# Performance work log

Hardware: AMD Instinct MI355X
Metric: run time of the kernel (lower is better)

Reference implementation:

```python
import jax, jax.numpy as jnp
import numpy as np

D_MODEL = 1024
D_FF = 4096
NUM_EXPERTS = 8
TOP_K = 2
SEQ = 1024
BATCH = 2


def setup_inputs() -> dict:
    key = jax.random.key(0)
    ks = jax.random.split(key, 7)
    s = 0.02
    x = jax.random.normal(ks[0], (SEQ, BATCH, D_MODEL), dtype=jnp.float32)
    gate_w = jax.random.normal(ks[1], (D_MODEL, NUM_EXPERTS), dtype=jnp.float32) * s
    gate_b = jnp.zeros((NUM_EXPERTS,), dtype=jnp.float32)
    W1 = jax.random.normal(ks[2], (NUM_EXPERTS, D_MODEL, D_FF), dtype=jnp.float32) * s
    b1 = jnp.zeros((NUM_EXPERTS, D_FF), dtype=jnp.float32)
    W2 = jax.random.normal(ks[3], (NUM_EXPERTS, D_FF, D_MODEL), dtype=jnp.float32) * s
    b2 = jnp.zeros((NUM_EXPERTS, D_MODEL), dtype=jnp.float32)
    return {"x": x, "gate_w": gate_w, "gate_b": gate_b,
            "W1": W1, "b1": b1, "W2": W2, "b2": b2}


def reference(x, gate_w, gate_b, W1, b1, W2, b2):
    S, B, D = x.shape
    x_flat = x.reshape(-1, D)                       # [T, D], T = S*B
    scores = x_flat @ gate_w + gate_b               # [T, E]
    topk_vals, topk_idx = jax.lax.top_k(scores, TOP_K)   # [T, K]
    topk_probs = jax.nn.softmax(topk_vals, axis=-1)      # [T, K]
    # combine weight per (token, expert): sum of probs over slots routed to e
    one_hot = jax.nn.one_hot(topk_idx, NUM_EXPERTS, dtype=x.dtype)  # [T, K, E]
    combine = jnp.einsum('tk,tke->te', topk_probs, one_hot)         # [T, E]
    # dense per-expert FFN (tokens with combine weight 0 contribute nothing,
    # matching the masked gather/scatter in the torch loop)
    h = jax.nn.relu(jnp.einsum('td,edf->etf', x_flat, W1) + b1[:, None, :])  # [E, T, F]
    y = jnp.einsum('etf,efd->etd', h, W2) + b2[:, None, :]                    # [E, T, D]
    out = jnp.einsum('te,etd->td', combine, y)       # [T, D]
    return out.reshape(S, B, D)
```

## Files before the change

kernel.cpp:

```cpp
#include <hip/hip_runtime.h>
#include <stdint.h>

#define T_TOKENS 2048
#define DM 1024
#define DF 4096
#define NEXP 8
#define NSLOTS (T_TOKENS * 2)

typedef __bf16 bf16x8 __attribute__((ext_vector_type(8)));
typedef float f32x4 __attribute__((ext_vector_type(4)));

__device__ __forceinline__ ushort f2bf(float f) {
    union { float f; uint32_t u; } v; v.f = f;
    uint32_t r = v.u + 0x7FFFu + ((v.u >> 16) & 1u);
    return (ushort)(r >> 16);
}

__device__ __forceinline__ void gload16(const ushort* g, ushort* l) {
    __builtin_amdgcn_global_load_lds(
        (const __attribute__((address_space(1))) uint32_t*)g,
        (__attribute__((address_space(3))) uint32_t*)l,
        16, 0, 0);
}

__global__ void init_cnt(uint32_t* cnt) {
    if (threadIdx.x < NEXP) cnt[threadIdx.x] = 0;
}

__global__ __launch_bounds__(256) void gate_route(
    const float* __restrict__ x, const float* __restrict__ gw,
    const float* __restrict__ gb,
    uint32_t* __restrict__ route, uint32_t* __restrict__ cnt,
    float* __restrict__ prob, uint32_t* __restrict__ epk)
{
    const int w = threadIdx.x >> 6;
    const int lane = threadIdx.x & 63;
    const int t = blockIdx.x * 4 + w;
    float acc[NEXP];
#pragma unroll
    for (int e = 0; e < NEXP; ++e) acc[e] = 0.f;
    const float* xr = x + (size_t)t * DM;
#pragma unroll
    for (int j = 0; j < DM / 64; ++j) {
        const int d = j * 64 + lane;
        const float xv = xr[d];
        const float* g = gw + (size_t)d * NEXP;
#pragma unroll
        for (int e = 0; e < NEXP; ++e) acc[e] += xv * g[e];
    }
#pragma unroll
    for (int e = 0; e < NEXP; ++e) {
#pragma unroll
        for (int off = 32; off > 0; off >>= 1)
            acc[e] += __shfl_xor(acc[e], off);
        acc[e] += gb[e];
    }
    if (lane == 0) {
        int e0 = 0; float v0 = acc[0];
#pragma unroll
        for (int e = 1; e < NEXP; ++e) if (acc[e] > v0) { v0 = acc[e]; e0 = e; }
        int e1 = -1; float v1 = -1e30f;
#pragma unroll
        for (int e = 0; e < NEXP; ++e) if (e != e0 && acc[e] > v1) { v1 = acc[e]; e1 = e; }
        const float ex = expf(v1 - v0);
        const float inv = 1.f / (1.f + ex);
        prob[t * 2 + 0] = inv;
        prob[t * 2 + 1] = ex * inv;
        uint32_t pos = atomicAdd(&cnt[e0], 1u);
        route[e0 * T_TOKENS + pos] = (uint32_t)(t * 2);
        epk[t * 2] = ((uint32_t)e0 << 16) | pos;
        pos = atomicAdd(&cnt[e1], 1u);
        route[e1 * T_TOKENS + pos] = (uint32_t)(t * 2 + 1);
        epk[t * 2 + 1] = ((uint32_t)e1 << 16) | pos;
    }
}

__global__ void prefix_offs(const uint32_t* __restrict__ cnt,
                            uint32_t* __restrict__ offs)
{
    if (threadIdx.x == 0) {
        uint32_t a = 0;
#pragma unroll
        for (int e = 0; e < NEXP; ++e) { offs[e] = a; a += cnt[e]; }
        offs[NEXP] = a;
    }
}

__global__ __launch_bounds__(256) void convert_x(const float* __restrict__ x,
                                                 ushort* __restrict__ xb)
{
    const int i = (blockIdx.x * 256 + threadIdx.x) * 4;
    const float4 v = *reinterpret_cast<const float4*>(x + i);
    ushort4 o;
    o.x = f2bf(v.x); o.y = f2bf(v.y); o.z = f2bf(v.z); o.w = f2bf(v.w);
    *reinterpret_cast<ushort4*>(xb + i) = o;
}

template<int K, int N>
__global__ __launch_bounds__(256) void conv_transpose(const float* __restrict__ W,
                                                      ushort* __restrict__ Wb)
{
    const int e  = blockIdx.y;
    const int nt = blockIdx.x % (N / 64);
    const int kt = blockIdx.x / (N / 64);
    const int k0 = kt * 64, n0 = nt * 64;
    __shared__ ushort T[64][80];
    const int t = threadIdx.x;
    const int kr = t >> 4, nc = (t & 15) * 4;
    const float* src = W + ((size_t)e * K + k0 + kr) * N + n0 + nc;
#pragma unroll
    for (int i = 0; i < 4; ++i) {
        const float4 v = *reinterpret_cast<const float4*>(src + (size_t)i * 16 * N);
        T[nc + 0][kr + i * 16] = f2bf(v.x);
        T[nc + 1][kr + i * 16] = f2bf(v.y);
        T[nc + 2][kr + i * 16] = f2bf(v.z);
        T[nc + 3][kr + i * 16] = f2bf(v.w);
    }
    __syncthreads();
    const int r = t >> 2, c0 = t & 3;
    ushort* dst = Wb + ((size_t)e * N + n0 + r) * K + k0;
#pragma unroll
    for (int i = 0; i < 2; ++i) {
        const int c = c0 + i * 4;
        const uint4 v = *reinterpret_cast<const uint4*>(&T[r][c * 8]);
        *reinterpret_cast<uint4*>(dst + c * 8) = v;
    }
}

template<int KD, int ND, bool FIRST, int SPLIT, int NMT, int NT>
__global__ __launch_bounds__(256, 4) void moe_gemm10(
    const ushort* __restrict__ Abuf,
    const ushort* __restrict__ Wb,
    const float* __restrict__ bias,
    const uint32_t* __restrict__ route,
    const uint32_t* __restrict__ cnt,
    const uint32_t* __restrict__ offs,
    const float* __restrict__ prob,
    ushort* __restrict__ hout,
    float* __restrict__ yout)
{
    const int bx0 = blockIdx.x;
    const int cpx = (NEXP * NMT * NT) >> 3;
    const int wk  = (bx0 & 7) * cpx + (bx0 >> 3);
    const int e   = wk / (NMT * NT);
    const int r   = wk % (NMT * NT);
    const int nt  = r / NMT;
    const int mt  = r % NMT;
    const uint32_t cntE = cnt[e];
    const int m0 = mt * 128;
    if ((uint32_t)m0 >= cntE) return;
    const uint32_t hb = offs[e];
    const int n0 = nt * 128;
    const int z  = (SPLIT > 1) ? (int)blockIdx.z : 0;
    const int kbeg = z * (KD / SPLIT);
    const int niter = (KD / SPLIT) / 32;

    __shared__ ushort As[2][128 * 32];
    __shared__ ushort Bs[2][128 * 32];
    __shared__ uint32_t s_route[128];
    __shared__ float s_p[128];

    const int tid = threadIdx.x;
    if (FIRST) {
        if (tid < 128) {
            const uint32_t idx = (uint32_t)(m0 + tid);
            const uint32_t s = (idx < cntE) ? route[e * T_TOKENS + idx] : 0u;
            s_route[tid] = s;
            s_p[tid] = prob[s];
        }
        __syncthreads();
    }

    const int w = tid >> 6, l = tid & 63;

    const ushort* asrc[2];
    const ushort* bsrc[2];
#pragma unroll
    for (int i = 0; i < 2; ++i) {
        const int chunk = (w * 2 + i) * 64 + l;
        const int row = chunk >> 2;
        const int c   = chunk & 3;
        const int cs  = c ^ ((row >> 1) & 3);
        size_t arow;
        if (FIRST) arow = (size_t)(s_route[row] >> 1);
        else       arow = (size_t)(hb + m0 + row);
        asrc[i] = Abuf + arow * KD + cs * 8 + kbeg;
        bsrc[i] = Wb + ((size_t)e * ND + n0 + row) * KD + cs * 8 + kbeg;
    }

    f32x4 acc[4][4];
#pragma unroll
    for (int i = 0; i < 4; ++i)
#pragma unroll
        for (int j = 0; j < 4; ++j) acc[i][j] = (f32x4){0.f, 0.f, 0.f, 0.f};

    const int q = l & 15, g = l >> 4;
    const int wm = w >> 1, wn = w & 1;

    int aoff[4], boff[4];
#pragma unroll
    for (int mi = 0; mi < 4; ++mi) {
        int row = wm * 64 + mi * 16 + q;
        aoff[mi] = row * 64 + (g ^ ((row >> 1) & 3)) * 16;
        row = wn * 64 + mi * 16 + q;
        boff[mi] = row * 64 + (g ^ ((row >> 1) & 3)) * 16;
    }

    ushort* const abase0 = &As[0][0];
    ushort* const bbase0 = &Bs[0][0];

#pragma unroll
    for (int i = 0; i < 2; ++i) gload16(asrc[i], abase0 + (w * 2 + i) * 512);
#pragma unroll
    for (int i = 0; i < 2; ++i) gload16(bsrc[i], bbase0 + (w * 2 + i) * 512);

    int cur = 0;
    for (int t = 0; t < niter; ++t) {
        if (t + 1 < niter) {
            ushort* ad = abase0 + (cur ^ 1) * (128 * 32) + (w * 2) * 512;
            ushort* bd = bbase0 + (cur ^ 1) * (128 * 32) + (w * 2) * 512;
            const int k1 = (t + 1) * 32;
#pragma unroll
            for (int i = 0; i < 2; ++i) gload16(asrc[i] + k1, ad + i * 512);
#pragma unroll
            for (int i = 0; i < 2; ++i) gload16(bsrc[i] + k1, bd + i * 512);
            asm volatile("s_waitcnt vmcnt(4)" ::: "memory");
        } else {
            asm volatile("s_waitcnt vmcnt(0)" ::: "memory");
        }
        __builtin_amdgcn_s_barrier();
        __builtin_amdgcn_sched_barrier(0);

        const char* Ab = (const char*)(abase0 + cur * (128 * 32));
        const char* Bb = (const char*)(bbase0 + cur * (128 * 32));
        bf16x8 af[4], bv[4];
#pragma unroll
        for (int mi = 0; mi < 4; ++mi)
            af[mi] = *reinterpret_cast<const bf16x8*>(Ab + aoff[mi]);
#pragma unroll
        for (int ni = 0; ni < 4; ++ni)
            bv[ni] = *reinterpret_cast<const bf16x8*>(Bb + boff[ni]);
        __builtin_amdgcn_s_setprio(1);
#pragma unroll
        for (int mi = 0; mi < 4; ++mi)
#pragma unroll
            for (int ni = 0; ni < 4; ++ni)
                acc[mi][ni] = __builtin_amdgcn_mfma_f32_16x16x32_bf16(
                    af[mi], bv[ni], acc[mi][ni], 0, 0, 0);
        __builtin_amdgcn_s_setprio(0);
        __builtin_amdgcn_s_barrier();
        cur ^= 1;
    }

#pragma unroll
    for (int mi = 0; mi < 4; ++mi) {
#pragma unroll
        for (int ni = 0; ni < 4; ++ni) {
            const int gcol = n0 + wn * 64 + ni * 16 + q;
#pragma unroll
            for (int j = 0; j < 4; ++j) {
                const int row = wm * 64 + mi * 16 + g * 4 + j;
                if ((uint32_t)(m0 + row) < cntE) {
                    const size_t grow = (size_t)(hb + m0 + row);
                    if (FIRST) {
                        float v = acc[mi][ni][j] + bias[e * ND + gcol];
                        v = fmaxf(v, 0.f) * s_p[row];
                        hout[grow * ND + gcol] = f2bf(v);
                    } else {
                        yout[((size_t)z * NSLOTS + grow) * ND + gcol] = acc[mi][ni][j];
                    }
                }
            }
        }
    }
}

__global__ __launch_bounds__(256) void combine5(
    const float* __restrict__ yc, const uint32_t* __restrict__ epk,
    const uint32_t* __restrict__ offs, const float* __restrict__ prob,
    const float* __restrict__ b2, float* __restrict__ out)
{
    const int gid = blockIdx.x * 256 + threadIdx.x;
    const int t = gid >> 8;
    const int dq = gid & 255;
    const uint32_t p0 = epk[2 * t], p1 = epk[2 * t + 1];
    const uint32_t e0 = p0 >> 16, e1 = p1 >> 16;
    const uint32_t r0 = offs[e0] + (p0 & 0xFFFFu);
    const uint32_t r1 = offs[e1] + (p1 & 0xFFFFu);
    const float w0 = prob[2 * t], w1 = prob[2 * t + 1];
    const float4 bb0 = reinterpret_cast<const float4*>(b2 + (size_t)e0 * DM)[dq];
    const float4 bb1 = reinterpret_cast<const float4*>(b2 + (size_t)e1 * DM)[dq];
    float4 o = { w0 * bb0.x + w1 * bb1.x, w0 * bb0.y + w1 * bb1.y,
                 w0 * bb0.z + w1 * bb1.z, w0 * bb0.w + w1 * bb1.w };
    const float4* Y = reinterpret_cast<const float4*>(yc);
#pragma unroll
    for (int zz = 0; zz < 4; ++zz) {
        const float4 a = Y[((size_t)zz * NSLOTS + r0) * 256 + dq];
        const float4 b = Y[((size_t)zz * NSLOTS + r1) * 256 + dq];
        o.x += a.x + b.x; o.y += a.y + b.y; o.z += a.z + b.z; o.w += a.w + b.w;
    }
    reinterpret_cast<float4*>(out)[gid] = o;
}

template<int KD, int ND, bool FIRST>
__global__ __launch_bounds__(256) void moe_gemm_v1(
    const ushort* __restrict__ Abuf, const float* __restrict__ W,
    const float* __restrict__ bias, const uint32_t* __restrict__ route,
    const uint32_t* __restrict__ cnt, const float* __restrict__ prob,
    ushort* __restrict__ hout, float* __restrict__ yout)
{
    const int e = blockIdx.x >> 4;
    const int mt = blockIdx.x & 15;
    const uint32_t cntE = cnt[e];
    const int m0 = mt * 128;
    if ((uint32_t)m0 >= cntE) return;
    const int n0 = blockIdx.y * 128;
    const int tid = threadIdx.x;
    __shared__ ushort Asm[128][40];
    __shared__ ushort Bsm[128][40];
    __shared__ uint32_t s_route[128];
    if (tid < 128) {
        const uint32_t idx = (uint32_t)(m0 + tid);
        s_route[tid] = (idx < cntE) ? route[e * T_TOKENS + idx] : 0xFFFFFFFFu;
    }
    __syncthreads();
    const int ar = tid >> 1, ah = tid & 1;
    const uint32_t s_a = s_route[ar];
    size_t arow = 0;
    if (s_a != 0xFFFFFFFFu) arow = FIRST ? (size_t)(s_a >> 1) : (size_t)s_a;
    const ushort* asrc = Abuf + arow * KD + ah * 16;
    const int c4 = tid & 31, kq = tid >> 5;
    const float* wbase = W + (size_t)e * KD * ND + (size_t)n0 + (size_t)c4 * 4;
    f32x4 acc[4][4];
#pragma unroll
    for (int i = 0; i < 4; ++i)
#pragma unroll
        for (int j = 0; j < 4; ++j) acc[i][j] = (f32x4){0.f, 0.f, 0.f, 0.f};
    const int lane = tid & 63, wv = tid >> 6;
    const int wm = wv >> 1, wn = wv & 1;
    const int q = lane & 15, g = lane >> 4;
    for (int k0 = 0; k0 < KD; k0 += 32) {
        {
            const uint4* src = reinterpret_cast<const uint4*>(asrc + k0);
            const uint4 v0 = src[0];
            const uint4 v1 = src[1];
            *reinterpret_cast<uint4*>(&Asm[ar][ah * 16]) = v0;
            *reinterpret_cast<uint4*>(&Asm[ar][ah * 16 + 8]) = v1;
        }
        {
            ushort vals[4][4];
#pragma unroll
            for (int r = 0; r < 4; ++r) {
                const float4 v = *reinterpret_cast<const float4*>(
                    wbase + (size_t)(k0 + kq * 4 + r) * ND);
                vals[r][0] = f2bf(v.x); vals[r][1] = f2bf(v.y);
                vals[r][2] = f2bf(v.z); vals[r][3] = f2bf(v.w);
            }
#pragma unroll
            for (int c = 0; c < 4; ++c) {
                const ushort4 o = { vals[0][c], vals[1][c], vals[2][c], vals[3][c] };
                *reinterpret_cast<ushort4*>(&Bsm[c4 * 4 + c][kq * 4]) = o;
            }
        }
        __syncthreads();
        bf16x8 af[4], bfr[4];
#pragma unroll
        for (int mi = 0; mi < 4; ++mi)
            af[mi] = *reinterpret_cast<const bf16x8*>(&Asm[wm * 64 + mi * 16 + q][g * 8]);
#pragma unroll
        for (int ni = 0; ni < 4; ++ni)
            bfr[ni] = *reinterpret_cast<const bf16x8*>(&Bsm[wn * 64 + ni * 16 + q][g * 8]);
#pragma unroll
        for (int mi = 0; mi < 4; ++mi)
#pragma unroll
            for (int ni = 0; ni < 4; ++ni)
                acc[mi][ni] = __builtin_amdgcn_mfma_f32_16x16x32_bf16(
                    af[mi], bfr[ni], acc[mi][ni], 0, 0, 0);
        __syncthreads();
    }
#pragma unroll
    for (int mi = 0; mi < 4; ++mi) {
#pragma unroll
        for (int ni = 0; ni < 4; ++ni) {
            const int gcol = n0 + wn * 64 + ni * 16 + q;
#pragma unroll
            for (int j = 0; j < 4; ++j) {
                const int row = wm * 64 + mi * 16 + g * 4 + j;
                if ((uint32_t)(m0 + row) < cntE) {
                    const uint32_t s = s_route[row];
                    float v = acc[mi][ni][j] + bias[e * ND + gcol];
                    if (FIRST) {
                        v = fmaxf(v, 0.f);
                        hout[(size_t)s * ND + gcol] = f2bf(v);
                    } else {
                        yout[(size_t)s * ND + gcol] = v * prob[s];
                    }
                }
            }
        }
    }
}

__global__ __launch_bounds__(256) void combine1(const float* __restrict__ yc,
                                                float* __restrict__ out)
{
    const int gid = blockIdx.x * 256 + threadIdx.x;
    const int t = gid >> 8;
    const int dq = gid & 255;
    const float4 va = reinterpret_cast<const float4*>(yc)[(size_t)(2 * t) * 256 + dq];
    const float4 vb = reinterpret_cast<const float4*>(yc)[(size_t)(2 * t + 1) * 256 + dq];
    const float4 o = { va.x + vb.x, va.y + vb.y, va.z + vb.z, va.w + vb.w };
    reinterpret_cast<float4*>(out)[gid] = o;
}

extern "C" void kernel_launch(void* const* d_in, const int* in_sizes, int n_in,
                              void* d_out, int out_size, void* d_ws, size_t ws_size,
                              hipStream_t stream)
{
    const float* x  = (const float*)d_in[0];
    const float* gw = (const float*)d_in[1];
    const float* gb = (const float*)d_in[2];
    const float* W1 = (const float*)d_in[3];
    const float* b1 = (const float*)d_in[4];
    const float* W2 = (const float*)d_in[5];
    const float* b2 = (const float*)d_in[6];
    float* out = (float*)d_out;
    char* ws = (char*)d_ws;

    const size_t OFF_XB    = 0;
    const size_t OFF_H     = 4194304;
    const size_t OFF_ROUTE = 38797312;
    const size_t OFF_CNT   = 38862848;
    const size_t OFF_OFFS  = 38862912;
    const size_t OFF_PROB  = 38862976;
    const size_t OFF_EPK   = 38879360;
    const size_t OFF_W1B   = 41943040;
    const size_t OFF_W2B   = 109051904;
    const size_t OFF_YC    = OFF_W1B;
    const size_t NEED      = 176160768ull;

    if (ws_size >= NEED) {
        ushort*   xb    = (ushort*)(ws + OFF_XB);
        ushort*   h     = (ushort*)(ws + OFF_H);
        float*    yc    = (float*)(ws + OFF_YC);
        uint32_t* route = (uint32_t*)(ws + OFF_ROUTE);
        uint32_t* cnt   = (uint32_t*)(ws + OFF_CNT);
        uint32_t* offs  = (uint32_t*)(ws + OFF_OFFS);
        float*    prob  = (float*)(ws + OFF_PROB);
        uint32_t* epk   = (uint32_t*)(ws + OFF_EPK);
        ushort*   w1b   = (ushort*)(ws + OFF_W1B);
        ushort*   w2b   = (ushort*)(ws + OFF_W2B);

        hipLaunchKernelGGL(init_cnt, dim3(1), dim3(64), 0, stream, cnt);
        hipLaunchKernelGGL(gate_route, dim3(T_TOKENS / 4), dim3(256), 0, stream,
                           x, gw, gb, route, cnt, prob, epk);
        hipLaunchKernelGGL(prefix_offs, dim3(1), dim3(64), 0, stream, cnt, offs);
        hipLaunchKernelGGL(convert_x, dim3(T_TOKENS * DM / 1024), dim3(256), 0, stream, x, xb);
        hipLaunchKernelGGL((conv_transpose<DM, DF>), dim3((DM / 64) * (DF / 64), NEXP),
                           dim3(256), 0, stream, W1, w1b);
        hipLaunchKernelGGL((moe_gemm10<DM, DF, true, 1, 16, 32>),
                           dim3(NEXP * 16 * 32, 1, 1), dim3(256), 0, stream,
                           xb, w1b, b1, route, cnt, offs, prob, h, (float*)nullptr);
        hipLaunchKernelGGL((conv_transpose<DF, DM>), dim3((DF / 64) * (DM / 64), NEXP),
                           dim3(256), 0, stream, W2, w2b);
        hipLaunchKernelGGL((moe_gemm10<DF, DM, false, 4, 16, 8>),
                           dim3(NEXP * 16 * 8, 1, 4), dim3(256), 0, stream,
                           h, w2b, (const float*)nullptr, route, cnt, offs,
                           (const float*)nullptr, (ushort*)nullptr, yc);
        hipLaunchKernelGGL(combine5, dim3(T_TOKENS * DM / 1024), dim3(256), 0, stream,
                           yc, epk, offs, prob, b2, out);
    } else {
        const size_t F_XB = 0, F_H = 4194304, F_YC = 37748736;
        const size_t F_ROUTE = 54525952, F_CNT = 54591488, F_PROB = 54591552;
        ushort*   xb    = (ushort*)(ws + F_XB);
        ushort*   h     = (ushort*)(ws + F_H);
        float*    yc    = (float*)(ws + F_YC);
        uint32_t* route = (uint32_t*)(ws + F_ROUTE);
        uint32_t* cnt   = (uint32_t*)(ws + F_CNT);
        float*    prob  = (float*)(ws + F_PROB);
        uint32_t* epk   = (uint32_t*)(ws + F_PROB + 16384);

        hipLaunchKernelGGL(init_cnt, dim3(1), dim3(64), 0, stream, cnt);
        hipLaunchKernelGGL(gate_route, dim3(T_TOKENS / 4), dim3(256), 0, stream,
                           x, gw, gb, route, cnt, prob, epk);
        hipLaunchKernelGGL(convert_x, dim3(T_TOKENS * DM / 1024), dim3(256), 0, stream, x, xb);
        hipLaunchKernelGGL((moe_gemm_v1<DM, DF, true>), dim3(NEXP * 16, DF / 128),
                           dim3(256), 0, stream, xb, W1, b1, route, cnt, prob,
                           h, (float*)nullptr);
        hipLaunchKernelGGL((moe_gemm_v1<DF, DM, false>), dim3(NEXP * 16, DM / 128),
                           dim3(256), 0, stream, h, W2, b2, route, cnt, prob,
                           (ushort*)nullptr, yc);
        hipLaunchKernelGGL(combine1, dim3(T_TOKENS * DM / 1024), dim3(256), 0, stream, yc, out);
    }
}
```

Before: 298.0 us.

## Merge gating, x/W1 conversion into one prep kernel; overlap W2 transpose with GEMM1

Gating/routing, the x-to-bf16 conversion and the W1 convert-transpose now run as one heterogeneous prep kernel whose block ranges are dispatched by block index. The W2 convert-transpose blocks are appended to the first expert GEMM's grid so they can fill idle compute units while GEMM1 runs. This removes several launches and the serialization between independent preprocessing stages. The cost is a larger shared-memory footprint for the mixed kernel, possible occupancy interference with the GEMM blocks, and transpose blocks that each loop over four k-tiles.

```diff
diff --git a/kernel.cpp b/kernel.cpp
--- a/kernel.cpp
+++ b/kernel.cpp
@@ -27,54 +27,6 @@
     if (threadIdx.x < NEXP) cnt[threadIdx.x] = 0;
 }
 
-__global__ __launch_bounds__(256) void gate_route(
-    const float* __restrict__ x, const float* __restrict__ gw,
-    const float* __restrict__ gb,
-    uint32_t* __restrict__ route, uint32_t* __restrict__ cnt,
-    float* __restrict__ prob, uint32_t* __restrict__ epk)
-{
-    const int w = threadIdx.x >> 6;
-    const int lane = threadIdx.x & 63;
-    const int t = blockIdx.x * 4 + w;
-    float acc[NEXP];
-#pragma unroll
-    for (int e = 0; e < NEXP; ++e) acc[e] = 0.f;
-    const float* xr = x + (size_t)t * DM;
-#pragma unroll
-    for (int j = 0; j < DM / 64; ++j) {
-        const int d = j * 64 + lane;
-        const float xv = xr[d];
-        const float* g = gw + (size_t)d * NEXP;
-#pragma unroll
-        for (int e = 0; e < NEXP; ++e) acc[e] += xv * g[e];
-    }
-#pragma unroll
-    for (int e = 0; e < NEXP; ++e) {
-#pragma unroll
-        for (int off = 32; off > 0; off >>= 1)
-            acc[e] += __shfl_xor(acc[e], off);
-        acc[e] += gb[e];
-    }
-    if (lane == 0) {
-        int e0 = 0; float v0 = acc[0];
-#pragma unroll
-        for (int e = 1; e < NEXP; ++e) if (acc[e] > v0) { v0 = acc[e]; e0 = e; }
-        int e1 = -1; float v1 = -1e30f;
-#pragma unroll
-        for (int e = 0; e < NEXP; ++e) if (e != e0 && acc[e] > v1) { v1 = acc[e]; e1 = e; }
-        const float ex = expf(v1 - v0);
-        const float inv = 1.f / (1.f + ex);
-        prob[t * 2 + 0] = inv;
-        prob[t * 2 + 1] = ex * inv;
-        uint32_t pos = atomicAdd(&cnt[e0], 1u);
-        route[e0 * T_TOKENS + pos] = (uint32_t)(t * 2);
-        epk[t * 2] = ((uint32_t)e0 << 16) | pos;
-        pos = atomicAdd(&cnt[e1], 1u);
-        route[e1 * T_TOKENS + pos] = (uint32_t)(t * 2 + 1);
-        epk[t * 2 + 1] = ((uint32_t)e1 << 16) | pos;
-    }
-}
-
 __global__ void prefix_offs(const uint32_t* __restrict__ cnt,
                             uint32_t* __restrict__ offs)
 {
@@ -86,44 +38,257 @@
     }
 }
 
-__global__ __launch_bounds__(256) void convert_x(const float* __restrict__ x,
-                                                 ushort* __restrict__ xb)
-{
-    const int i = (blockIdx.x * 256 + threadIdx.x) * 4;
-    const float4 v = *reinterpret_cast<const float4*>(x + i);
-    ushort4 o;
-    o.x = f2bf(v.x); o.y = f2bf(v.y); o.z = f2bf(v.z); o.w = f2bf(v.w);
-    *reinterpret_cast<ushort4*>(xb + i) = o;
-}
-
-template<int K, int N>
-__global__ __launch_bounds__(256) void conv_transpose(const float* __restrict__ W,
-                                                      ushort* __restrict__ Wb)
-{
-    const int e  = blockIdx.y;
-    const int nt = blockIdx.x % (N / 64);
-    const int kt = blockIdx.x / (N / 64);
-    const int k0 = kt * 64, n0 = nt * 64;
+__global__ __launch_bounds__(256) void prep_kernel(
+    const float* __restrict__ x, const float* __restrict__ gw,
+    const float* __restrict__ gb, const float* __restrict__ W1,
+    uint32_t* __restrict__ route, uint32_t* __restrict__ cnt,
+    float* __restrict__ prob, uint32_t* __restrict__ epk,
+    ushort* __restrict__ xb, ushort* __restrict__ w1b)
+{
     __shared__ ushort T[64][80];
-    const int t = threadIdx.x;
-    const int kr = t >> 4, nc = (t & 15) * 4;
-    const float* src = W + ((size_t)e * K + k0 + kr) * N + n0 + nc;
-#pragma unroll
-    for (int i = 0; i < 4; ++i) {
-        const float4 v = *reinterpret_cast<const float4*>(src + (size_t)i * 16 * N);
-        T[nc + 0][kr + i * 16] = f2bf(v.x);
-        T[nc + 1][kr + i * 16] = f2bf(v.y);
-        T[nc + 2][kr + i * 16] = f2bf(v.z);
-        T[nc + 3][kr + i * 16] = f2bf(v.w);
-    }
-    __syncthreads();
-    const int r = t >> 2, c0 = t & 3;
-    ushort* dst = Wb + ((size_t)e * N + n0 + r) * K + k0;
-#pragma unroll
-    for (int i = 0; i < 2; ++i) {
-        const int c = c0 + i * 4;
-        const uint4 v = *reinterpret_cast<const uint4*>(&T[r][c * 8]);
-        *reinterpret_cast<uint4*>(dst + c * 8) = v;
+    const int bx = blockIdx.x;
+    const int tid = threadIdx.x;
+
+    if (bx < 512) {
+        const int w = tid >> 6;
+        const int lane = tid & 63;
+        const int t = bx * 4 + w;
+        float acc[NEXP];
+#pragma unroll
+        for (int e = 0; e < NEXP; ++e) acc[e] = 0.f;
+        const float* xr = x + (size_t)t * DM;
+#pragma unroll
+        for (int j = 0; j < DM / 64; ++j) {
+            const int d = j * 64 + lane;
+            const float xv = xr[d];
+            const float* g = gw + (size_t)d * NEXP;
+#pragma unroll
+            for (int e = 0; e < NEXP; ++e) acc[e] += xv * g[e];
+        }
+#pragma unroll
+        for (int e = 0; e < NEXP; ++e) {
+#pragma unroll
+            for (int off = 32; off > 0; off >>= 1)
+                acc[e] += __shfl_xor(acc[e], off);
+            acc[e] += gb[e];
+        }
+        if (lane == 0) {
+            int e0 = 0; float v0 = acc[0];
+#pragma unroll
+            for (int e = 1; e < NEXP; ++e) if (acc[e] > v0) { v0 = acc[e]; e0 = e; }
+            int e1 = -1; float v1 = -1e30f;
+#pragma unroll
+            for (int e = 0; e < NEXP; ++e) if (e != e0 && acc[e] > v1) { v1 = acc[e]; e1 = e; }
+            const float ex = expf(v1 - v0);
+            const float inv = 1.f / (1.f + ex);
+            prob[t * 2 + 0] = inv;
+            prob[t * 2 + 1] = ex * inv;
+            uint32_t pos = atomicAdd(&cnt[e0], 1u);
+            route[e0 * T_TOKENS + pos] = (uint32_t)(t * 2);
+            epk[t * 2] = ((uint32_t)e0 << 16) | pos;
+            pos = atomicAdd(&cnt[e1], 1u);
+            route[e1 * T_TOKENS + pos] = (uint32_t)(t * 2 + 1);
+            epk[t * 2 + 1] = ((uint32_t)e1 << 16) | pos;
+        }
+    } else if (bx < 2560) {
+        const int i = ((bx - 512) * 256 + tid) * 4;
+        const float4 v = *reinterpret_cast<const float4*>(x + i);
+        ushort4 o;
+        o.x = f2bf(v.x); o.y = f2bf(v.y); o.z = f2bf(v.z); o.w = f2bf(v.w);
+        *reinterpret_cast<ushort4*>(xb + i) = o;
+    } else {
+        const int rel = bx - 2560;
+        const int e   = rel >> 8;
+        const int r   = rel & 255;
+        const int nt  = r & 63;
+        const int ktg = r >> 6;
+        const int kr  = tid >> 4, nc = (tid & 15) * 4;
+        const int rr  = tid >> 2, c0 = tid & 3;
+        for (int kk = 0; kk < 4; ++kk) {
+            const int k0 = ktg * 256 + kk * 64;
+            const int n0 = nt * 64;
+            const float* src = W1 + ((size_t)e * DM + k0 + kr) * DF + n0 + nc;
+#pragma unroll
+            for (int i2 = 0; i2 < 4; ++i2) {
+                const float4 v = *reinterpret_cast<const float4*>(src + (size_t)i2 * 16 * DF);
+                T[nc + 0][kr + i2 * 16] = f2bf(v.x);
+                T[nc + 1][kr + i2 * 16] = f2bf(v.y);
+                T[nc + 2][kr + i2 * 16] = f2bf(v.z);
+                T[nc + 3][kr + i2 * 16] = f2bf(v.w);
+            }
+            __syncthreads();
+            ushort* dst = w1b + ((size_t)e * DF + n0 + rr) * DM + k0;
+#pragma unroll
+            for (int i2 = 0; i2 < 2; ++i2) {
+                const int c = c0 + i2 * 4;
+                *reinterpret_cast<uint4*>(dst + c * 8) =
+                    *reinterpret_cast<const uint4*>(&T[rr][c * 8]);
+            }
+            __syncthreads();
+        }
+    }
+}
+
+__global__ __launch_bounds__(256, 4) void gemm1_trw2(
+    const ushort* __restrict__ xb, const ushort* __restrict__ w1b,
+    const float* __restrict__ b1, const uint32_t* __restrict__ route,
+    const uint32_t* __restrict__ cnt, const uint32_t* __restrict__ offs,
+    const float* __restrict__ prob, ushort* __restrict__ hout,
+    const float* __restrict__ W2, ushort* __restrict__ w2b)
+{
+    __shared__ __attribute__((aligned(16))) char smem[33792];
+    const int bx0 = blockIdx.x;
+    const int tid = threadIdx.x;
+
+    if (bx0 < 4096) {
+        ushort* Asm = (ushort*)smem;
+        ushort* Bsm = (ushort*)(smem + 16384);
+        uint32_t* s_route = (uint32_t*)(smem + 32768);
+        float* s_p = (float*)(smem + 33280);
+
+        const int cpx = (NEXP * 16 * 32) >> 3;
+        const int wk  = (bx0 & 7) * cpx + (bx0 >> 3);
+        const int e   = wk / (16 * 32);
+        const int r   = wk % (16 * 32);
+        const int nt  = r / 16;
+        const int mt  = r % 16;
+        const uint32_t cntE = cnt[e];
+        const int m0 = mt * 128;
+        if ((uint32_t)m0 >= cntE) return;
+        const uint32_t hb = offs[e];
+        const int n0 = nt * 128;
+        const int niter = DM / 32;
+
+        if (tid < 128) {
+            const uint32_t idx = (uint32_t)(m0 + tid);
+            const uint32_t s = (idx < cntE) ? route[e * T_TOKENS + idx] : 0u;
+            s_route[tid] = s;
+            s_p[tid] = prob[s];
+        }
+        __syncthreads();
+
+        const int w = tid >> 6, l = tid & 63;
+        const ushort* asrc[2];
+        const ushort* bsrc[2];
+#pragma unroll
+        for (int i = 0; i < 2; ++i) {
+            const int chunk = (w * 2 + i) * 64 + l;
+            const int row = chunk >> 2;
+            const int c   = chunk & 3;
+            const int cs  = c ^ ((row >> 1) & 3);
+            const size_t arow = (size_t)(s_route[row] >> 1);
+            asrc[i] = xb + arow * DM + cs * 8;
+            bsrc[i] = w1b + ((size_t)e * DF + n0 + row) * DM + cs * 8;
+        }
+
+        f32x4 acc[4][4];
+#pragma unroll
+        for (int i = 0; i < 4; ++i)
+#pragma unroll
+            for (int j = 0; j < 4; ++j) acc[i][j] = (f32x4){0.f, 0.f, 0.f, 0.f};
+
+        const int q = l & 15, g = l >> 4;
+        const int wm = w >> 1, wn = w & 1;
+        int aoff[4], boff[4];
+#pragma unroll
+        for (int mi = 0; mi < 4; ++mi) {
+            int row = wm * 64 + mi * 16 + q;
+            aoff[mi] = row * 64 + (g ^ ((row >> 1) & 3)) * 16;
+            row = wn * 64 + mi * 16 + q;
+            boff[mi] = row * 64 + (g ^ ((row >> 1) & 3)) * 16;
+        }
+
+#pragma unroll
+        for (int i = 0; i < 2; ++i) gload16(asrc[i], Asm + (w * 2 + i) * 512);
+#pragma unroll
+        for (int i = 0; i < 2; ++i) gload16(bsrc[i], Bsm + (w * 2 + i) * 512);
+
+        int cur = 0;
+        for (int t = 0; t < niter; ++t) {
+            if (t + 1 < niter) {
+                ushort* ad = Asm + (cur ^ 1) * (128 * 32) + (w * 2) * 512;
+                ushort* bd = Bsm + (cur ^ 1) * (128 * 32) + (w * 2) * 512;
+                const int k1 = (t + 1) * 32;
+#pragma unroll
+                for (int i = 0; i < 2; ++i) gload16(asrc[i] + k1, ad + i * 512);
+#pragma unroll
+                for (int i = 0; i < 2; ++i) gload16(bsrc[i] + k1, bd + i * 512);
+                asm volatile("s_waitcnt vmcnt(4)" ::: "memory");
+            } else {
+                asm volatile("s_waitcnt vmcnt(0)" ::: "memory");
+            }
+            __builtin_amdgcn_s_barrier();
+            __builtin_amdgcn_sched_barrier(0);
+
+            const char* Ab = (const char*)(Asm + cur * (128 * 32));
+            const char* Bb = (const char*)(Bsm + cur * (128 * 32));
+            bf16x8 af[4], bv[4];
+#pragma unroll
+            for (int mi = 0; mi < 4; ++mi)
+                af[mi] = *reinterpret_cast<const bf16x8*>(Ab + aoff[mi]);
+#pragma unroll
+            for (int ni = 0; ni < 4; ++ni)
+                bv[ni] = *reinterpret_cast<const bf16x8*>(Bb + boff[ni]);
+            __builtin_amdgcn_s_setprio(1);
+#pragma unroll
+            for (int mi = 0; mi < 4; ++mi)
+#pragma unroll
+                for (int ni = 0; ni < 4; ++ni)
+                    acc[mi][ni] = __builtin_amdgcn_mfma_f32_16x16x32_bf16(
+                        af[mi], bv[ni], acc[mi][ni], 0, 0, 0);
+            __builtin_amdgcn_s_setprio(0);
+            __builtin_amdgcn_s_barrier();
+            cur ^= 1;
+        }
+
+#pragma unroll
+        for (int mi = 0; mi < 4; ++mi) {
+#pragma unroll
+            for (int ni = 0; ni < 4; ++ni) {
+                const int gcol = n0 + wn * 64 + ni * 16 + q;
+#pragma unroll
+                for (int j = 0; j < 4; ++j) {
+                    const int row = wm * 64 + mi * 16 + g * 4 + j;
+                    if ((uint32_t)(m0 + row) < cntE) {
+                        const size_t grow = (size_t)(hb + m0 + row);
+                        float v = acc[mi][ni][j] + b1[e * DF + gcol];
+                        v = fmaxf(v, 0.f) * s_p[row];
+                        hout[grow * DF + gcol] = f2bf(v);
+                    }
+                }
+            }
+        }
+    } else {
+        ushort (*T)[80] = reinterpret_cast<ushort(*)[80]>(smem);
+        const int rel = bx0 - 4096;
+        const int e   = rel >> 8;
+        const int r   = rel & 255;
+        const int nt  = r & 15;
+        const int ktg = r >> 4;
+        const int kr  = tid >> 4, nc = (tid & 15) * 4;
+        const int rr  = tid >> 2, c0 = tid & 3;
+        for (int kk = 0; kk < 4; ++kk) {
+            const int k0 = ktg * 256 + kk * 64;
+            const int n0 = nt * 64;
+            const float* src = W2 + ((size_t)e * DF + k0 + kr) * DM + n0 + nc;
+#pragma unroll
+            for (int i2 = 0; i2 < 4; ++i2) {
+                const float4 v = *reinterpret_cast<const float4*>(src + (size_t)i2 * 16 * DM);
+                T[nc + 0][kr + i2 * 16] = f2bf(v.x);
+                T[nc + 1][kr + i2 * 16] = f2bf(v.y);
+                T[nc + 2][kr + i2 * 16] = f2bf(v.z);
+                T[nc + 3][kr + i2 * 16] = f2bf(v.w);
+            }
+            __syncthreads();
+            ushort* dst = w2b + ((size_t)e * DM + n0 + rr) * DF + k0;
+#pragma unroll
+            for (int i2 = 0; i2 < 2; ++i2) {
+                const int c = c0 + i2 * 4;
+                *reinterpret_cast<uint4*>(dst + c * 8) =
+                    *reinterpret_cast<const uint4*>(&T[rr][c * 8]);
+            }
+            __syncthreads();
+        }
     }
 }
 
@@ -172,7 +337,6 @@
     }
 
     const int w = tid >> 6, l = tid & 63;
-
     const ushort* asrc[2];
     const ushort* bsrc[2];
 #pragma unroll
@@ -196,7 +360,6 @@
 
     const int q = l & 15, g = l >> 4;
     const int wm = w >> 1, wn = w & 1;
-
     int aoff[4], boff[4];
 #pragma unroll
     for (int mi = 0; mi < 4; ++mi) {
@@ -302,6 +465,62 @@
     reinterpret_cast<float4*>(out)[gid] = o;
 }
 
+__global__ __launch_bounds__(256) void gate_route_fb(
+    const float* __restrict__ x, const float* __restrict__ gw,
+    const float* __restrict__ gb,
+    uint32_t* __restrict__ route, uint32_t* __restrict__ cnt,
+    float* __restrict__ prob)
+{
+    const int w = threadIdx.x >> 6;
+    const int lane = threadIdx.x & 63;
+    const int t = blockIdx.x * 4 + w;
+    float acc[NEXP];
+#pragma unroll
+    for (int e = 0; e < NEXP; ++e) acc[e] = 0.f;
+    const float* xr = x + (size_t)t * DM;
+#pragma unroll
+    for (int j = 0; j < DM / 64; ++j) {
+        const int d = j * 64 + lane;
+        const float xv = xr[d];
+        const float* g = gw + (size_t)d * NEXP;
+#pragma unroll
+        for (int e = 0; e < NEXP; ++e) acc[e] += xv * g[e];
+    }
+#pragma unroll
+    for (int e = 0; e < NEXP; ++e) {
+#pragma unroll
+        for (int off = 32; off > 0; off >>= 1)
+            acc[e] += __shfl_xor(acc[e], off);
+        acc[e] += gb[e];
+    }
+    if (lane == 0) {
+        int e0 = 0; float v0 = acc[0];
+#pragma unroll
+        for (int e = 1; e < NEXP; ++e) if (acc[e] > v0) { v0 = acc[e]; e0 = e; }
+        int e1 = -1; float v1 = -1e30f;
+#pragma unroll
+        for (int e = 0; e < NEXP; ++e) if (e != e0 && acc[e] > v1) { v1 = acc[e]; e1 = e; }
+        const float ex = expf(v1 - v0);
+        const float inv = 1.f / (1.f + ex);
+        prob[t * 2 + 0] = inv;
+        prob[t * 2 + 1] = ex * inv;
+        uint32_t pos = atomicAdd(&cnt[e0], 1u);
+        route[e0 * T_TOKENS + pos] = (uint32_t)(t * 2);
+        pos = atomicAdd(&cnt[e1], 1u);
+        route[e1 * T_TOKENS + pos] = (uint32_t)(t * 2 + 1);
+    }
+}
+
+__global__ __launch_bounds__(256) void convert_x_fb(const float* __restrict__ x,
+                                                    ushort* __restrict__ xb)
+{
+    const int i = (blockIdx.x * 256 + threadIdx.x) * 4;
+    const float4 v = *reinterpret_cast<const float4*>(x + i);
+    ushort4 o;
+    o.x = f2bf(v.x); o.y = f2bf(v.y); o.z = f2bf(v.z); o.w = f2bf(v.w);
+    *reinterpret_cast<ushort4*>(xb + i) = o;
+}
+
 template<int KD, int ND, bool FIRST>
 __global__ __launch_bounds__(256) void moe_gemm_v1(
     const ushort* __restrict__ Abuf, const float* __restrict__ W,
@@ -452,17 +671,11 @@
         ushort*   w2b   = (ushort*)(ws + OFF_W2B);
 
         hipLaunchKernelGGL(init_cnt, dim3(1), dim3(64), 0, stream, cnt);
-        hipLaunchKernelGGL(gate_route, dim3(T_TOKENS / 4), dim3(256), 0, stream,
-                           x, gw, gb, route, cnt, prob, epk);
+        hipLaunchKernelGGL(prep_kernel, dim3(4608), dim3(256), 0, stream,
+                           x, gw, gb, W1, route, cnt, prob, epk, xb, w1b);
         hipLaunchKernelGGL(prefix_offs, dim3(1), dim3(64), 0, stream, cnt, offs);
-        hipLaunchKernelGGL(convert_x, dim3(T_TOKENS * DM / 1024), dim3(256), 0, stream, x, xb);
-        hipLaunchKernelGGL((conv_transpose<DM, DF>), dim3((DM / 64) * (DF / 64), NEXP),
-                           dim3(256), 0, stream, W1, w1b);
-        hipLaunchKernelGGL((moe_gemm10<DM, DF, true, 1, 16, 32>),
-                           dim3(NEXP * 16 * 32, 1, 1), dim3(256), 0, stream,
-                           xb, w1b, b1, route, cnt, offs, prob, h, (float*)nullptr);
-        hipLaunchKernelGGL((conv_transpose<DF, DM>), dim3((DF / 64) * (DM / 64), NEXP),
-                           dim3(256), 0, stream, W2, w2b);
+        hipLaunchKernelGGL(gemm1_trw2, dim3(4096 + 2048), dim3(256), 0, stream,
+                           xb, w1b, b1, route, cnt, offs, prob, h, W2, w2b);
         hipLaunchKernelGGL((moe_gemm10<DF, DM, false, 4, 16, 8>),
                            dim3(NEXP * 16 * 8, 1, 4), dim3(256), 0, stream,
                            h, w2b, (const float*)nullptr, route, cnt, offs,
@@ -478,12 +691,11 @@
         uint32_t* route = (uint32_t*)(ws + F_ROUTE);
         uint32_t* cnt   = (uint32_t*)(ws + F_CNT);
         float*    prob  = (float*)(ws + F_PROB);
-        uint32_t* epk   = (uint32_t*)(ws + F_PROB + 16384);
 
         hipLaunchKernelGGL(init_cnt, dim3(1), dim3(64), 0, stream, cnt);
-        hipLaunchKernelGGL(gate_route, dim3(T_TOKENS / 4), dim3(256), 0, stream,
-                           x, gw, gb, route, cnt, prob, epk);
-        hipLaunchKernelGGL(convert_x, dim3(T_TOKENS * DM / 1024), dim3(256), 0, stream, x, xb);
+        hipLaunchKernelGGL(gate_route_fb, dim3(T_TOKENS / 4), dim3(256), 0, stream,
+                           x, gw, gb, route, cnt, prob);
+        hipLaunchKernelGGL(convert_x_fb, dim3(T_TOKENS * DM / 1024), dim3(256), 0, stream, x, xb);
         hipLaunchKernelGGL((moe_gemm_v1<DM, DF, true>), dim3(NEXP * 16, DF / 128),
                            dim3(256), 0, stream, xb, W1, b1, route, cnt, prob,
                            h, (float*)nullptr);
```

Result: faster. 285.9 us (-4.1%).

## Convert fp32 weights to bf16 inside GEMM loaders; fuse gating with x conversion

Applied to the files above, without the earlier changes.

Removes the separate conv_transpose kernels that wrote bf16 transposed copies of W1 and W2. The GEMM now reads the fp32 weights directly, converts and transposes them in registers, and writes them to a padded LDS buffer, prefetching one step ahead. Gate routing and x conversion are merged into one launch. This saves a full read and write of the weights per call, but the GEMM now reads twice as many weight bytes, does conversion work in the inner loop, and replaces the async global-to-LDS copy for B with register staging plus __syncthreads.

```diff
diff --git a/kernel.cpp b/kernel.cpp
--- a/kernel.cpp
+++ b/kernel.cpp
@@ -27,110 +27,81 @@
     if (threadIdx.x < NEXP) cnt[threadIdx.x] = 0;
 }
 
-__global__ __launch_bounds__(256) void gate_route(
+__global__ void prefix_offs(const uint32_t* __restrict__ cnt,
+                            uint32_t* __restrict__ offs)
+{
+    if (threadIdx.x == 0) {
+        uint32_t a = 0;
+#pragma unroll
+        for (int e = 0; e < NEXP; ++e) { offs[e] = a; a += cnt[e]; }
+        offs[NEXP] = a;
+    }
+}
+
+__global__ __launch_bounds__(256) void prep_kernel(
     const float* __restrict__ x, const float* __restrict__ gw,
     const float* __restrict__ gb,
     uint32_t* __restrict__ route, uint32_t* __restrict__ cnt,
-    float* __restrict__ prob, uint32_t* __restrict__ epk)
-{
-    const int w = threadIdx.x >> 6;
-    const int lane = threadIdx.x & 63;
-    const int t = blockIdx.x * 4 + w;
-    float acc[NEXP];
-#pragma unroll
-    for (int e = 0; e < NEXP; ++e) acc[e] = 0.f;
-    const float* xr = x + (size_t)t * DM;
-#pragma unroll
-    for (int j = 0; j < DM / 64; ++j) {
-        const int d = j * 64 + lane;
-        const float xv = xr[d];
-        const float* g = gw + (size_t)d * NEXP;
-#pragma unroll
-        for (int e = 0; e < NEXP; ++e) acc[e] += xv * g[e];
-    }
-#pragma unroll
-    for (int e = 0; e < NEXP; ++e) {
-#pragma unroll
-        for (int off = 32; off > 0; off >>= 1)
-            acc[e] += __shfl_xor(acc[e], off);
-        acc[e] += gb[e];
-    }
-    if (lane == 0) {
-        int e0 = 0; float v0 = acc[0];
-#pragma unroll
-        for (int e = 1; e < NEXP; ++e) if (acc[e] > v0) { v0 = acc[e]; e0 = e; }
-        int e1 = -1; float v1 = -1e30f;
-#pragma unroll
-        for (int e = 0; e < NEXP; ++e) if (e != e0 && acc[e] > v1) { v1 = acc[e]; e1 = e; }
-        const float ex = expf(v1 - v0);
-        const float inv = 1.f / (1.f + ex);
-        prob[t * 2 + 0] = inv;
-        prob[t * 2 + 1] = ex * inv;
-        uint32_t pos = atomicAdd(&cnt[e0], 1u);
-        route[e0 * T_TOKENS + pos] = (uint32_t)(t * 2);
-        epk[t * 2] = ((uint32_t)e0 << 16) | pos;
-        pos = atomicAdd(&cnt[e1], 1u);
-        route[e1 * T_TOKENS + pos] = (uint32_t)(t * 2 + 1);
-        epk[t * 2 + 1] = ((uint32_t)e1 << 16) | pos;
-    }
-}
-
-__global__ void prefix_offs(const uint32_t* __restrict__ cnt,
-                            uint32_t* __restrict__ offs)
-{
-    if (threadIdx.x == 0) {
-        uint32_t a = 0;
-#pragma unroll
-        for (int e = 0; e < NEXP; ++e) { offs[e] = a; a += cnt[e]; }
-        offs[NEXP] = a;
-    }
-}
-
-__global__ __launch_bounds__(256) void convert_x(const float* __restrict__ x,
-                                                 ushort* __restrict__ xb)
-{
-    const int i = (blockIdx.x * 256 + threadIdx.x) * 4;
-    const float4 v = *reinterpret_cast<const float4*>(x + i);
-    ushort4 o;
-    o.x = f2bf(v.x); o.y = f2bf(v.y); o.z = f2bf(v.z); o.w = f2bf(v.w);
-    *reinterpret_cast<ushort4*>(xb + i) = o;
-}
-
-template<int K, int N>
-__global__ __launch_bounds__(256) void conv_transpose(const float* __restrict__ W,
-                                                      ushort* __restrict__ Wb)
-{
-    const int e  = blockIdx.y;
-    const int nt = blockIdx.x % (N / 64);
-    const int kt = blockIdx.x / (N / 64);
-    const int k0 = kt * 64, n0 = nt * 64;
-    __shared__ ushort T[64][80];
-    const int t = threadIdx.x;
-    const int kr = t >> 4, nc = (t & 15) * 4;
-    const float* src = W + ((size_t)e * K + k0 + kr) * N + n0 + nc;
-#pragma unroll
-    for (int i = 0; i < 4; ++i) {
-        const float4 v = *reinterpret_cast<const float4*>(src + (size_t)i * 16 * N);
-        T[nc + 0][kr + i * 16] = f2bf(v.x);
-        T[nc + 1][kr + i * 16] = f2bf(v.y);
-        T[nc + 2][kr + i * 16] = f2bf(v.z);
-        T[nc + 3][kr + i * 16] = f2bf(v.w);
-    }
-    __syncthreads();
-    const int r = t >> 2, c0 = t & 3;
-    ushort* dst = Wb + ((size_t)e * N + n0 + r) * K + k0;
-#pragma unroll
-    for (int i = 0; i < 2; ++i) {
-        const int c = c0 + i * 4;
-        const uint4 v = *reinterpret_cast<const uint4*>(&T[r][c * 8]);
-        *reinterpret_cast<uint4*>(dst + c * 8) = v;
+    float* __restrict__ prob, uint32_t* __restrict__ epk,
+    ushort* __restrict__ xb)
+{
+    const int bx = blockIdx.x;
+    const int tid = threadIdx.x;
+
+    if (bx < 512) {
+        const int w = tid >> 6;
+        const int lane = tid & 63;
+        const int t = bx * 4 + w;
+        float acc[NEXP];
+#pragma unroll
+        for (int e = 0; e < NEXP; ++e) acc[e] = 0.f;
+        const float* xr = x + (size_t)t * DM;
+#pragma unroll
+        for (int j = 0; j < DM / 64; ++j) {
+            const int d = j * 64 + lane;
+            const float xv = xr[d];
+            const float* g = gw + (size_t)d * NEXP;
+#pragma unroll
+            for (int e = 0; e < NEXP; ++e) acc[e] += xv * g[e];
+        }
+#pragma unroll
+        for (int e = 0; e < NEXP; ++e) {
+#pragma unroll
+            for (int off = 32; off > 0; off >>= 1)
+                acc[e] += __shfl_xor(acc[e], off);
+            acc[e] += gb[e];
+        }
+        if (lane == 0) {
+            int e0 = 0; float v0 = acc[0];
+#pragma unroll
+            for (int e = 1; e < NEXP; ++e) if (acc[e] > v0) { v0 = acc[e]; e0 = e; }
+            int e1 = -1; float v1 = -1e30f;
+#pragma unroll
+            for (int e = 0; e < NEXP; ++e) if (e != e0 && acc[e] > v1) { v1 = acc[e]; e1 = e; }
+            const float ex = expf(v1 - v0);
+            const float inv = 1.f / (1.f + ex);
+            prob[t * 2 + 0] = inv;
+            prob[t * 2 + 1] = ex * inv;
+            uint32_t pos = atomicAdd(&cnt[e0], 1u);
+            route[e0 * T_TOKENS + pos] = (uint32_t)(t * 2);
+            epk[t * 2] = ((uint32_t)e0 << 16) | pos;
+            pos = atomicAdd(&cnt[e1], 1u);
+            route[e1 * T_TOKENS + pos] = (uint32_t)(t * 2 + 1);
+            epk[t * 2 + 1] = ((uint32_t)e1 << 16) | pos;
+        }
+    } else {
+        const int i = ((bx - 512) * 256 + tid) * 4;
+        const float4 v = *reinterpret_cast<const float4*>(x + i);
+        ushort4 o;
+        o.x = f2bf(v.x); o.y = f2bf(v.y); o.z = f2bf(v.z); o.w = f2bf(v.w);
+        *reinterpret_cast<ushort4*>(xb + i) = o;
     }
 }
 
 template<int KD, int ND, bool FIRST, int SPLIT, int NMT, int NT>
-__global__ __launch_bounds__(256, 4) void moe_gemm10(
+__global__ __launch_bounds__(256, 4) void moe_gemm12(
     const ushort* __restrict__ Abuf,
-    const ushort* __restrict__ Wb,
+    const float* __restrict__ W,
     const float* __restrict__ bias,
     const uint32_t* __restrict__ route,
     const uint32_t* __restrict__ cnt,
@@ -156,7 +127,7 @@
     const int niter = (KD / SPLIT) / 32;
 
     __shared__ ushort As[2][128 * 32];
-    __shared__ ushort Bs[2][128 * 32];
+    __shared__ ushort Bs[2][128 * 40];
     __shared__ uint32_t s_route[128];
     __shared__ float s_p[128];
 
@@ -174,7 +145,6 @@
     const int w = tid >> 6, l = tid & 63;
 
     const ushort* asrc[2];
-    const ushort* bsrc[2];
 #pragma unroll
     for (int i = 0; i < 2; ++i) {
         const int chunk = (w * 2 + i) * 64 + l;
@@ -185,8 +155,13 @@
         if (FIRST) arow = (size_t)(s_route[row] >> 1);
         else       arow = (size_t)(hb + m0 + row);
         asrc[i] = Abuf + arow * KD + cs * 8 + kbeg;
-        bsrc[i] = Wb + ((size_t)e * ND + n0 + row) * KD + cs * 8 + kbeg;
-    }
+    }
+
+    const int c4 = tid & 31;
+    const int kq = tid >> 5;
+    const float* wbase = W + ((size_t)e * KD + kbeg + (size_t)kq * 4) * ND
+                         + n0 + c4 * 4;
+    ushort* const bdst0 = &Bs[0][0];
 
     f32x4 acc[4][4];
 #pragma unroll
@@ -203,36 +178,47 @@
         int row = wm * 64 + mi * 16 + q;
         aoff[mi] = row * 64 + (g ^ ((row >> 1) & 3)) * 16;
         row = wn * 64 + mi * 16 + q;
-        boff[mi] = row * 64 + (g ^ ((row >> 1) & 3)) * 16;
+        boff[mi] = row * 40 + g * 8;
     }
 
     ushort* const abase0 = &As[0][0];
-    ushort* const bbase0 = &Bs[0][0];
-
-#pragma unroll
-    for (int i = 0; i < 2; ++i) gload16(asrc[i], abase0 + (w * 2 + i) * 512);
-#pragma unroll
-    for (int i = 0; i < 2; ++i) gload16(bsrc[i], bbase0 + (w * 2 + i) * 512);
+
+    {
+        float4 b0 = *reinterpret_cast<const float4*>(wbase + (size_t)0 * ND);
+        float4 b1 = *reinterpret_cast<const float4*>(wbase + (size_t)1 * ND);
+        float4 b2 = *reinterpret_cast<const float4*>(wbase + (size_t)2 * ND);
+        float4 b3 = *reinterpret_cast<const float4*>(wbase + (size_t)3 * ND);
+#pragma unroll
+        for (int i = 0; i < 2; ++i) gload16(asrc[i], abase0 + (w * 2 + i) * 512);
+        const int bn = c4 * 4;
+        ushort4 o0 = { f2bf(b0.x), f2bf(b1.x), f2bf(b2.x), f2bf(b3.x) };
+        ushort4 o1 = { f2bf(b0.y), f2bf(b1.y), f2bf(b2.y), f2bf(b3.y) };
+        ushort4 o2 = { f2bf(b0.z), f2bf(b1.z), f2bf(b2.z), f2bf(b3.z) };
+        ushort4 o3 = { f2bf(b0.w), f2bf(b1.w), f2bf(b2.w), f2bf(b3.w) };
+        *reinterpret_cast<ushort4*>(bdst0 + (bn + 0) * 40 + kq * 4) = o0;
+        *reinterpret_cast<ushort4*>(bdst0 + (bn + 1) * 40 + kq * 4) = o1;
+        *reinterpret_cast<ushort4*>(bdst0 + (bn + 2) * 40 + kq * 4) = o2;
+        *reinterpret_cast<ushort4*>(bdst0 + (bn + 3) * 40 + kq * 4) = o3;
+    }
+    __syncthreads();
 
     int cur = 0;
     for (int t = 0; t < niter; ++t) {
-        if (t + 1 < niter) {
+        float4 b0, b1, b2, b3;
+        const bool pf = (t + 1 < niter);
+        if (pf) {
+            const size_t k1 = (size_t)(t + 1) * 32;
+            b0 = *reinterpret_cast<const float4*>(wbase + (k1 + 0) * ND);
+            b1 = *reinterpret_cast<const float4*>(wbase + (k1 + 1) * ND);
+            b2 = *reinterpret_cast<const float4*>(wbase + (k1 + 2) * ND);
+            b3 = *reinterpret_cast<const float4*>(wbase + (k1 + 3) * ND);
             ushort* ad = abase0 + (cur ^ 1) * (128 * 32) + (w * 2) * 512;
-            ushort* bd = bbase0 + (cur ^ 1) * (128 * 32) + (w * 2) * 512;
-            const int k1 = (t + 1) * 32;
 #pragma unroll
             for (int i = 0; i < 2; ++i) gload16(asrc[i] + k1, ad + i * 512);
-#pragma unroll
-            for (int i = 0; i < 2; ++i) gload16(bsrc[i] + k1, bd + i * 512);
-            asm volatile("s_waitcnt vmcnt(4)" ::: "memory");
-        } else {
-            asm volatile("s_waitcnt vmcnt(0)" ::: "memory");
-        }
-        __builtin_amdgcn_s_barrier();
-        __builtin_amdgcn_sched_barrier(0);
+        }
 
         const char* Ab = (const char*)(abase0 + cur * (128 * 32));
-        const char* Bb = (const char*)(bbase0 + cur * (128 * 32));
+        const ushort* Bb = bdst0 + cur * (128 * 40);
         bf16x8 af[4], bv[4];
 #pragma unroll
         for (int mi = 0; mi < 4; ++mi)
@@ -248,7 +234,21 @@
                 acc[mi][ni] = __builtin_amdgcn_mfma_f32_16x16x32_bf16(
                     af[mi], bv[ni], acc[mi][ni], 0, 0, 0);
         __builtin_amdgcn_s_setprio(0);
-        __builtin_amdgcn_s_barrier();
+        __builtin_amdgcn_sched_barrier(0);
+
+        if (pf) {
+            ushort* bd = bdst0 + (cur ^ 1) * (128 * 40);
+            const int bn = c4 * 4;
+            ushort4 o0 = { f2bf(b0.x), f2bf(b1.x), f2bf(b2.x), f2bf(b3.x) };
+            ushort4 o1 = { f2bf(b0.y), f2bf(b1.y), f2bf(b2.y), f2bf(b3.y) };
+            ushort4 o2 = { f2bf(b0.z), f2bf(b1.z), f2bf(b2.z), f2bf(b3.z) };
+            ushort4 o3 = { f2bf(b0.w), f2bf(b1.w), f2bf(b2.w), f2bf(b3.w) };
+            *reinterpret_cast<ushort4*>(bd + (bn + 0) * 40 + kq * 4) = o0;
+            *reinterpret_cast<ushort4*>(bd + (bn + 1) * 40 + kq * 4) = o1;
+            *reinterpret_cast<ushort4*>(bd + (bn + 2) * 40 + kq * 4) = o2;
+            *reinterpret_cast<ushort4*>(bd + (bn + 3) * 40 + kq * 4) = o3;
+        }
+        __syncthreads();
         cur ^= 1;
     }
 
@@ -302,6 +302,62 @@
     reinterpret_cast<float4*>(out)[gid] = o;
 }
 
+__global__ __launch_bounds__(256) void gate_route_fb(
+    const float* __restrict__ x, const float* __restrict__ gw,
+    const float* __restrict__ gb,
+    uint32_t* __restrict__ route, uint32_t* __restrict__ cnt,
+    float* __restrict__ prob)
+{
+    const int w = threadIdx.x >> 6;
+    const int lane = threadIdx.x & 63;
+    const int t = blockIdx.x * 4 + w;
+    float acc[NEXP];
+#pragma unroll
+    for (int e = 0; e < NEXP; ++e) acc[e] = 0.f;
+    const float* xr = x + (size_t)t * DM;
+#pragma unroll
+    for (int j = 0; j < DM / 64; ++j) {
+        const int d = j * 64 + lane;
+        const float xv = xr[d];
+        const float* g = gw + (size_t)d * NEXP;
+#pragma unroll
+        for (int e = 0; e < NEXP; ++e) acc[e] += xv * g[e];
+    }
+#pragma unroll
+    for (int e = 0; e < NEXP; ++e) {
+#pragma unroll
+        for (int off = 32; off > 0; off >>= 1)
+            acc[e] += __shfl_xor(acc[e], off);
+        acc[e] += gb[e];
+    }
+    if (lane == 0) {
+        int e0 = 0; float v0 = acc[0];
+#pragma unroll
+        for (int e = 1; e < NEXP; ++e) if (acc[e] > v0) { v0 = acc[e]; e0 = e; }
+        int e1 = -1; float v1 = -1e30f;
+#pragma unroll
+        for (int e = 0; e < NEXP; ++e) if (e != e0 && acc[e] > v1) { v1 = acc[e]; e1 = e; }
+        const float ex = expf(v1 - v0);
+        const float inv = 1.f / (1.f + ex);
+        prob[t * 2 + 0] = inv;
+        prob[t * 2 + 1] = ex * inv;
+        uint32_t pos = atomicAdd(&cnt[e0], 1u);
+        route[e0 * T_TOKENS + pos] = (uint32_t)(t * 2);
+        pos = atomicAdd(&cnt[e1], 1u);
+        route[e1 * T_TOKENS + pos] = (uint32_t)(t * 2 + 1);
+    }
+}
+
+__global__ __launch_bounds__(256) void convert_x_fb(const float* __restrict__ x,
+                                                    ushort* __restrict__ xb)
+{
+    const int i = (blockIdx.x * 256 + threadIdx.x) * 4;
+    const float4 v = *reinterpret_cast<const float4*>(x + i);
+    ushort4 o;
+    o.x = f2bf(v.x); o.y = f2bf(v.y); o.z = f2bf(v.z); o.w = f2bf(v.w);
+    *reinterpret_cast<ushort4*>(xb + i) = o;
+}
+
 template<int KD, int ND, bool FIRST>
 __global__ __launch_bounds__(256) void moe_gemm_v1(
     const ushort* __restrict__ Abuf, const float* __restrict__ W,
@@ -434,10 +490,8 @@
     const size_t OFF_OFFS  = 38862912;
     const size_t OFF_PROB  = 38862976;
     const size_t OFF_EPK   = 38879360;
-    const size_t OFF_W1B   = 41943040;
-    const size_t OFF_W2B   = 109051904;
-    const size_t OFF_YC    = OFF_W1B;
-    const size_t NEED      = 176160768ull;
+    const size_t OFF_YC    = 41943040;
+    const size_t NEED      = 109051904ull;
 
     if (ws_size >= NEED) {
         ushort*   xb    = (ushort*)(ws + OFF_XB);
@@ -448,24 +502,17 @@
         uint32_t* offs  = (uint32_t*)(ws + OFF_OFFS);
         float*    prob  = (float*)(ws + OFF_PROB);
         uint32_t* epk   = (uint32_t*)(ws + OFF_EPK);
-        ushort*   w1b   = (ushort*)(ws + OFF_W1B);
-        ushort*   w2b   = (ushort*)(ws + OFF_W2B);
 
         hipLaunchKernelGGL(init_cnt, dim3(1), dim3(64), 0, stream, cnt);
-        hipLaunchKernelGGL(gate_route, dim3(T_TOKENS / 4), dim3(256), 0, stream,
-                           x, gw, gb, route, cnt, prob, epk);
+        hipLaunchKernelGGL(prep_kernel, dim3(2560), dim3(256), 0, stream,
+                           x, gw, gb, route, cnt, prob, epk, xb);
         hipLaunchKernelGGL(prefix_offs, dim3(1), dim3(64), 0, stream, cnt, offs);
-        hipLaunchKernelGGL(convert_x, dim3(T_TOKENS * DM / 1024), dim3(256), 0, stream, x, xb);
-        hipLaunchKernelGGL((conv_transpose<DM, DF>), dim3((DM / 64) * (DF / 64), NEXP),
-                           dim3(256), 0, stream, W1, w1b);
-        hipLaunchKernelGGL((moe_gemm10<DM, DF, true, 1, 16, 32>),
+        hipLaunchKernelGGL((moe_gemm12<DM, DF, true, 1, 16, 32>),
                            dim3(NEXP * 16 * 32, 1, 1), dim3(256), 0, stream,
-                           xb, w1b, b1, route, cnt, offs, prob, h, (float*)nullptr);
-        hipLaunchKernelGGL((conv_transpose<DF, DM>), dim3((DF / 64) * (DM / 64), NEXP),
-                           dim3(256), 0, stream, W2, w2b);
-        hipLaunchKernelGGL((moe_gemm10<DF, DM, false, 4, 16, 8>),
+                           xb, W1, b1, route, cnt, offs, prob, h, (float*)nullptr);
+        hipLaunchKernelGGL((moe_gemm12<DF, DM, false, 4, 16, 8>),
                            dim3(NEXP * 16 * 8, 1, 4), dim3(256), 0, stream,
-                           h, w2b, (const float*)nullptr, route, cnt, offs,
+                           h, W2, (const float*)nullptr, route, cnt, offs,
                            (const float*)nullptr, (ushort*)nullptr, yc);
         hipLaunchKernelGGL(combine5, dim3(T_TOKENS * DM / 1024), dim3(256), 0, stream,
                            yc, epk, offs, prob, b2, out);
@@ -478,12 +525,11 @@
         uint32_t* route = (uint32_t*)(ws + F_ROUTE);
         uint32_t* cnt   = (uint32_t*)(ws + F_CNT);
         float*    prob  = (float*)(ws + F_PROB);
-        uint32_t* epk   = (uint32_t*)(ws + F_PROB + 16384);
 
         hipLaunchKernelGGL(init_cnt, dim3(1), dim3(64), 0, stream, cnt);
-        hipLaunchKernelGGL(gate_route, dim3(T_TOKENS / 4), dim3(256), 0, stream,
-                           x, gw, gb, route, cnt, prob, epk);
-        hipLaunchKernelGGL(convert_x, dim3(T_TOKENS * DM / 1024), dim3(256), 0, stream, x, xb);
+        hipLaunchKernelGGL(gate_route_fb, dim3(T_TOKENS / 4), dim3(256), 0, stream,
+                           x, gw, gb, route, cnt, prob);
+        hipLaunchKernelGGL(convert_x_fb, dim3(T_TOKENS * DM / 1024), dim3(256), 0, stream, x, xb);
         hipLaunchKernelGGL((moe_gemm_v1<DM, DF, true>), dim3(NEXP * 16, DF / 128),
                            dim3(256), 0, stream, xb, W1, b1, route, cnt, prob,
                            h, (float*)nullptr);
```

Measured after the change: 338.2 us. 13.5% more time.
